# Kernel tuning notes

Measured on AMD Instinct MI355X. Metric: run time of the kernel, lower is better.

The kernel has to match this reference:

```python
import jax, jax.numpy as jnp
import numpy as np
from math import sqrt

B, T, C, H = 4, 2048, 1024, 16
D = C // H  # head dim = 64


def setup_inputs() -> dict:
    key = jax.random.key(0)
    ks = jax.random.split(key, 9)
    s = 1.0 / sqrt(C)
    return {
        "x": jax.random.normal(ks[0], (B, T, C), dtype=jnp.float32),
        "Wk": jax.random.normal(ks[1], (C, C), dtype=jnp.float32) * s,
        "bk": jax.random.normal(ks[2], (C,), dtype=jnp.float32) * 0.01,
        "Wq": jax.random.normal(ks[3], (C, C), dtype=jnp.float32) * s,
        "bq": jax.random.normal(ks[4], (C,), dtype=jnp.float32) * 0.01,
        "Wv": jax.random.normal(ks[5], (C, C), dtype=jnp.float32) * s,
        "bv": jax.random.normal(ks[6], (C,), dtype=jnp.float32) * 0.01,
        "Wp": jax.random.normal(ks[7], (C, C), dtype=jnp.float32) * s,
        "bp": jax.random.normal(ks[8], (C,), dtype=jnp.float32) * 0.01,
    }


def reference(x, Wk, bk, Wq, bq, Wv, bv, Wp, bp):
    # Linear projections, split into heads: [B, H, T, D]
    def heads(y):
        return y.reshape(B, T, H, D).transpose(0, 2, 1, 3)

    k = heads(x @ Wk + bk)
    q = heads(x @ Wq + bq)
    v = heads(x @ Wv + bv)

    # scaled dot-product attention with causal mask (dropout p=0 -> identity)
    attn = jnp.einsum("bhtd,bhsd->bhts", q, k) / jnp.sqrt(jnp.float32(D))
    causal = jnp.tril(jnp.ones((T, T), dtype=bool))
    attn = jnp.where(causal[None, None], attn, -jnp.inf)
    attn = jax.nn.softmax(attn, axis=-1)

    y = jnp.einsum("bhts,bhsd->bhtd", attn, v)  # [B, H, T, D]
    y = y.transpose(0, 2, 1, 3).reshape(B, T, C)
    return y @ Wp + bp
```

## Files before the change

### kernel.cpp

```cpp
#include <hip/hip_runtime.h>
#include <hip/hip_bf16.h>
#include <math.h>


typedef short bf16x8 __attribute__((ext_vector_type(8)));
typedef float f32x4 __attribute__((ext_vector_type(4)));
typedef _Float16 f16x4 __attribute__((ext_vector_type(4)));

__device__ __forceinline__ short f2b(float f) {
    unsigned u = __float_as_uint(f);
    u = (u + 0x7fffu + ((u >> 16) & 1u)) >> 16;
    return (short)u;
}
__device__ __forceinline__ float b2f(short s) {
    return __uint_as_float(((unsigned)(unsigned short)s) << 16);
}

__global__ __launch_bounds__(256) void cast_x_kernel(const float* __restrict__ x,
                                                     short* __restrict__ xb, int n4) {
    int idx = blockIdx.x * 256 + threadIdx.x;
    if (idx >= n4) return;
    float4 v = ((const float4*)x)[idx];
    short4 o;
    o.x = f2b(v.x); o.y = f2b(v.y); o.z = f2b(v.z); o.w = f2b(v.w);
    ((short4*)xb)[idx] = o;
}

__global__ __launch_bounds__(256) void wtrans_kernel(const float* W0, const float* W1,
                                                     const float* W2, const float* W3,
                                                     short* O0, short* O1, short* O2, short* O3) {
    const float* W; short* O;
    switch (blockIdx.z) {
        case 0: W = W0; O = O0; break;
        case 1: W = W1; O = O1; break;
        case 2: W = W2; O = O2; break;
        default: W = W3; O = O3; break;
    }
    __shared__ __align__(16) float Ls[64 * 68];
    int tid = threadIdx.x;
    int n0 = blockIdx.x * 64, k0 = blockIdx.y * 64;
    #pragma unroll
    for (int it = 0; it < 4; ++it) {
        int c = tid + it * 256;
        int r = c >> 4, off = (c & 15) * 4;
        *(float4*)&Ls[r * 68 + off] = *(const float4*)&W[(k0 + r) * 1024 + n0 + off];
    }
    __syncthreads();
    #pragma unroll
    for (int it = 0; it < 2; ++it) {
        int c = tid + it * 256;
        int n = c >> 3, koff = (c & 7) * 8;
        union { short s[8]; int4 v; } u;
        #pragma unroll
        for (int k = 0; k < 8; ++k) u.s[k] = f2b(Ls[(koff + k) * 68 + n]);
        *(int4*)&O[(n0 + n) * 1024 + k0 + koff] = u.v;
    }
}

template<int MODE>
__global__ __launch_bounds__(512, 2) void gemm8_kernel(const short* __restrict__ A,
                                                       const short* Bt0, const short* Bt1, const short* Bt2,
                                                       const float* b0, const float* b1, const float* b2,
                                                       float s0, float s1, float s2,
                                                       void* O0, void* O1, void* O2) {
    int z = blockIdx.z;
    const short* Bt   = (z == 0) ? Bt0 : (z == 1) ? Bt1 : Bt2;
    const float* bias = (z == 0) ? b0  : (z == 1) ? b1  : b2;
    float scl         = (z == 0) ? s0  : (z == 1) ? s1  : s2;
    void* Out         = (z == 0) ? O0  : (z == 1) ? O1  : O2;

    __shared__ __align__(16) short lds[73728];

    int tid = threadIdx.x;
    int w = tid >> 6, lane = tid & 63, quad = lane >> 4, l15 = lane & 15;
    int m0 = blockIdx.x * 128, n0 = blockIdx.y * 256;

    int srccol = ((lane & 3) * 8) ^ ((lane & 32) ? 16 : 0);
    const short* pA0 = A  + (m0 + w * 16 + (lane >> 2)) * 1024 + srccol;
    const short* pA1 = pA0 + 32;
    const short* pB0 = Bt + (n0 + (2 * w) * 16 + (lane >> 2)) * 1024 + srccol;
    const short* pB1 = pB0 + 32;
    const short* pB2 = pB0 + 16 * 1024;
    const short* pB3 = pB2 + 32;

    int dA = (w * 2) * 512;
    int dB = 24576 + (w * 4) * 512;

    int offR = l15 * 64 + ((quad * 16) ^ ((l15 & 8) << 2));
    int ma4 = (w >> 2) * 4;
    int nb2 = (w & 3) * 2;
    const char* ldsb = (const char*)lds;

    f32x4 acc[2][4][2] = {};

#define STG(p, off) __builtin_amdgcn_global_load_lds( \
        (const __attribute__((address_space(1))) unsigned int*)(p), \
        (__attribute__((address_space(3))) unsigned int*)&lds[off], 16, 0, 0)

    STG(pA0,      dA);                 STG(pA1,      dA + 512);
    STG(pB0,      dB);                 STG(pB1,      dB + 512);
    STG(pB2,      dB + 1024);          STG(pB3,      dB + 1536);
    STG(pA0 + 64, 8192 + dA);          STG(pA1 + 64, 8192 + dA + 512);
    STG(pB0 + 64, 16384 + dB);         STG(pB1 + 64, 16384 + dB + 512);
    STG(pB2 + 64, 16384 + dB + 1024);  STG(pB3 + 64, 16384 + dB + 1536);
    asm volatile("s_waitcnt vmcnt(6)" ::: "memory");
    __builtin_amdgcn_s_barrier();
    __builtin_amdgcn_sched_barrier(0);

    #pragma unroll
    for (int t = 0; t < 16; ++t) {
        const int rs = t % 3;
        const int ss = (t + 2) % 3;
        const int Ar = rs * 16384;
        const int Br = 49152 + rs * 32768;

        bf16x8 af[4][2], bf[2][2];
        #pragma unroll
        for (int i = 0; i < 4; ++i)
            #pragma unroll
            for (int kk = 0; kk < 2; ++kk)
                af[i][kk] = *(const bf16x8*)(ldsb + Ar + ((ma4 + i) * 2 + kk) * 1024 + offR);
        #pragma unroll
        for (int j = 0; j < 2; ++j)
            #pragma unroll
            for (int kk = 0; kk < 2; ++kk)
                bf[j][kk] = *(const bf16x8*)(ldsb + Br + ((nb2 + j) * 2 + kk) * 1024 + offR);
        if (t + 2 < 16) {
            STG(pA0 + (t + 2) * 64, ss * 8192 + dA);
            STG(pA1 + (t + 2) * 64, ss * 8192 + dA + 512);
            STG(pB0 + (t + 2) * 64, ss * 16384 + dB);
        }
        __builtin_amdgcn_s_barrier();
        asm volatile("s_waitcnt lgkmcnt(0)" ::: "memory");
        __builtin_amdgcn_sched_barrier(0);
        __builtin_amdgcn_s_setprio(1);
        #pragma unroll
        for (int i = 0; i < 4; ++i)
            #pragma unroll
            for (int j = 0; j < 2; ++j) {
                acc[0][i][j] = __builtin_amdgcn_mfma_f32_16x16x32_bf16(af[i][0], bf[j][0], acc[0][i][j], 0, 0, 0);
                acc[0][i][j] = __builtin_amdgcn_mfma_f32_16x16x32_bf16(af[i][1], bf[j][1], acc[0][i][j], 0, 0, 0);
            }
        __builtin_amdgcn_s_setprio(0);
        __builtin_amdgcn_s_barrier();
        __builtin_amdgcn_sched_barrier(0);

        #pragma unroll
        for (int j = 0; j < 2; ++j)
            #pragma unroll
            for (int kk = 0; kk < 2; ++kk)
                bf[j][kk] = *(const bf16x8*)(ldsb + Br + ((8 + nb2 + j) * 2 + kk) * 1024 + offR);
        if (t + 2 < 16) {
            STG(pB1 + (t + 2) * 64, ss * 16384 + dB + 512);
            STG(pB2 + (t + 2) * 64, ss * 16384 + dB + 1024);
            STG(pB3 + (t + 2) * 64, ss * 16384 + dB + 1536);
        }
        __builtin_amdgcn_s_barrier();
        asm volatile("s_waitcnt lgkmcnt(0)" ::: "memory");
        __builtin_amdgcn_sched_barrier(0);
        __builtin_amdgcn_s_setprio(1);
        #pragma unroll
        for (int i = 0; i < 4; ++i)
            #pragma unroll
            for (int j = 0; j < 2; ++j) {
                acc[1][i][j] = __builtin_amdgcn_mfma_f32_16x16x32_bf16(af[i][0], bf[j][0], acc[1][i][j], 0, 0, 0);
                acc[1][i][j] = __builtin_amdgcn_mfma_f32_16x16x32_bf16(af[i][1], bf[j][1], acc[1][i][j], 0, 0, 0);
            }
        __builtin_amdgcn_s_setprio(0);
        if (t < 14) {
            asm volatile("s_waitcnt vmcnt(6)" ::: "memory");
        } else if (t == 14) {
            asm volatile("s_waitcnt vmcnt(0)" ::: "memory");
        }
        if (t < 15) {
            __builtin_amdgcn_s_barrier();
            __builtin_amdgcn_sched_barrier(0);
        }
    }
#undef STG

    int mrow = m0 + (w >> 2) * 64;
    int ncol = n0 + (w & 3) * 32;
    #pragma unroll
    for (int nh = 0; nh < 2; ++nh) {
        #pragma unroll
        for (int i = 0; i < 4; ++i) {
            #pragma unroll
            for (int j = 0; j < 2; ++j) {
                int gn = ncol + nh * 128 + j * 16 + l15;
                float bv = bias[gn];
                #pragma unroll
                for (int r = 0; r < 4; ++r) {
                    int gm = mrow + i * 16 + quad * 4 + r;
                    float v = (acc[nh][i][j][r] + bv) * scl;
                    if (MODE == 0) {
                        int b = gm >> 11, tt = gm & 2047, h = gn >> 6, d = gn & 63;
                        ((short*)Out)[(((b * 16 + h) * 2048) + tt) * 64 + d] = f2b(v);
                    } else {
                        ((float*)Out)[gm * 1024 + gn] = v;
                    }
                }
            }
        }
    }
}

__global__ __launch_bounds__(256) void vtrans_kernel(const short* __restrict__ V,
                                                     _Float16* __restrict__ Vt) {
    __shared__ __align__(16) short Ts[64 * 72];
    int tid = threadIdx.x;
    int bh = blockIdx.y;
    int t0 = blockIdx.x * 64;
    #pragma unroll
    for (int it = 0; it < 2; ++it) {
        int c = tid + it * 256;
        int r = c >> 3, off = (c & 7) * 8;
        *(int4*)&Ts[r * 72 + off] = *(const int4*)&V[(bh * 2048 + t0 + r) * 64 + off];
    }
    __syncthreads();
    #pragma unroll
    for (int it = 0; it < 2; ++it) {
        int c = tid + it * 256;
        int d = c >> 3, toff = (c & 7) * 8;
        union { _Float16 h[8]; int4 v; } u;
        #pragma unroll
        for (int k = 0; k < 8; ++k) u.h[k] = (_Float16)b2f(Ts[(toff + k) * 72 + d]);
        *(int4*)&Vt[(bh * 64 + d) * 2048 + t0 + toff] = u.v;
    }
}

__global__ __launch_bounds__(256, 3) void attn_kernel(const short* __restrict__ Q,
                                                      const short* __restrict__ K,
                                                      const _Float16* __restrict__ Vt,
                                                      short* __restrict__ Y) {
    __shared__ __align__(16) short    Ks[128 * 64];
    __shared__ __align__(16) _Float16 Vs[64 * 128];

    int tid = threadIdx.x;
    int w = tid >> 6, lane = tid & 63, quad = lane >> 4, l15 = lane & 15;
    int idx = blockIdx.x;
    int qi = 15 - (idx >> 6);
    int bh = idx & 63;

    const short* Qh = Q + bh * 2048 * 64;
    const short* Kh = K + bh * 2048 * 64;
    const _Float16* Vh = Vt + bh * 64 * 2048;

    bf16x8 qf[2][2];
    #pragma unroll
    for (int i = 0; i < 2; ++i)
        #pragma unroll
        for (int kh = 0; kh < 2; ++kh) {
            int t = qi * 128 + w * 32 + i * 16 + l15;
            qf[i][kh] = *(const bf16x8*)&Qh[t * 64 + kh * 32 + quad * 8];
        }

    int krow = lane >> 3;
    int kchunk = ((lane & 7) ^ krow) * 8;
    int vrow = lane >> 4;
    int vchunk = ((lane & 15) ^ (w * 4 + vrow)) * 8;

    int t7 = l15 & 7;
    int kf0_off = ((quad ^ t7) * 8);
    int kf1_off = (((quad + 4) ^ t7) * 8);
    int vsub = (quad & 1) * 4;
    int vchi = quad >> 1;

    f32x4 o[2][4] = {};
    float lsum[2] = {0.f, 0.f};

    for (int si = 0; si <= qi; ++si) {
        const short* Kt = Kh + si * 128 * 64;
        const _Float16* Vtile = Vh + si * 128;
        bool diag = (si == qi);

        __syncthreads();
        #pragma unroll
        for (int it = 0; it < 4; ++it) {
            int kr0 = it * 32 + w * 8;
            __builtin_amdgcn_global_load_lds(
                (const __attribute__((address_space(1))) unsigned int*)&Kt[(kr0 + krow) * 64 + kchunk],
                (__attribute__((address_space(3))) unsigned int*)&Ks[kr0 * 64], 16, 0, 0);
            int vr0 = it * 16 + w * 4;
            __builtin_amdgcn_global_load_lds(
                (const __attribute__((address_space(1))) unsigned int*)&Vtile[(vr0 + vrow) * 2048 + vchunk],
                (__attribute__((address_space(3))) unsigned int*)&Vs[vr0 * 128], 16, 0, 0);
        }
        __syncthreads();

        #pragma unroll
        for (int j = 0; j < 8; ++j) {
            int trow = (j * 16 + l15) * 64;
            bf16x8 kf0 = *(const bf16x8*)&Ks[trow + kf0_off];
            bf16x8 kf1 = *(const bf16x8*)&Ks[trow + kf1_off];
            f16x4 pfv[2];
            #pragma unroll
            for (int i = 0; i < 2; ++i) {
                f32x4 a = {};
                a = __builtin_amdgcn_mfma_f32_16x16x32_bf16(kf0, qf[i][0], a, 0, 0, 0);
                a = __builtin_amdgcn_mfma_f32_16x16x32_bf16(kf1, qf[i][1], a, 0, 0, 0);
                if (diag) {
                    int qrel = w * 32 + i * 16 + l15;
                    #pragma unroll
                    for (int r = 0; r < 4; ++r)
                        if (j * 16 + quad * 4 + r > qrel) a[r] = -1e30f;
                }
                float p0 = __builtin_amdgcn_exp2f(a[0]);
                float p1 = __builtin_amdgcn_exp2f(a[1]);
                float p2 = __builtin_amdgcn_exp2f(a[2]);
                float p3 = __builtin_amdgcn_exp2f(a[3]);
                lsum[i] += (p0 + p1) + (p2 + p3);
                pfv[i][0] = (_Float16)p0;
                pfv[i][1] = (_Float16)p1;
                pfv[i][2] = (_Float16)p2;
                pfv[i][3] = (_Float16)p3;
            }
            int vc = (j * 2 + vchi);
            #pragma unroll
            for (int mt = 0; mt < 4; ++mt) {
                int d = mt * 16 + l15;
                f16x4 vf = *(const f16x4*)&Vs[d * 128 + ((vc ^ l15) * 8) + vsub];
                o[0][mt] = __builtin_amdgcn_mfma_f32_16x16x16f16(vf, pfv[0], o[0][mt], 0, 0, 0);
                o[1][mt] = __builtin_amdgcn_mfma_f32_16x16x16f16(vf, pfv[1], o[1][mt], 0, 0, 0);
            }
        }
    }

    int b = bh >> 4, h = bh & 15;
    #pragma unroll
    for (int i = 0; i < 2; ++i) {
        float l = lsum[i];
        l += __shfl_xor(l, 16);
        l += __shfl_xor(l, 32);
        float rinv = 1.0f / l;
        int q = qi * 128 + w * 32 + i * 16 + l15;
        short* yrow = &Y[(b * 2048 + q) * 1024 + h * 64];
        #pragma unroll
        for (int mt = 0; mt < 4; ++mt) {
            short4 s4;
            s4.x = f2b(o[i][mt][0] * rinv);
            s4.y = f2b(o[i][mt][1] * rinv);
            s4.z = f2b(o[i][mt][2] * rinv);
            s4.w = f2b(o[i][mt][3] * rinv);
            *(short4*)&yrow[mt * 16 + quad * 4] = s4;
        }
    }
}

extern "C" void kernel_launch(void* const* d_in, const int* in_sizes, int n_in,
                              void* d_out, int out_size, void* d_ws, size_t ws_size,
                              hipStream_t stream) {
    const float* x  = (const float*)d_in[0];
    const float* Wk = (const float*)d_in[1];
    const float* bk = (const float*)d_in[2];
    const float* Wq = (const float*)d_in[3];
    const float* bq = (const float*)d_in[4];
    const float* Wv = (const float*)d_in[5];
    const float* bv = (const float*)d_in[6];
    const float* Wp = (const float*)d_in[7];
    const float* bp = (const float*)d_in[8];

    char* ws = (char*)d_ws;
    short*     xb  = (short*)(ws + 0);
    short*     Wqt = (short*)(ws + 16777216);
    short*     Wkt = (short*)(ws + 18874368);
    short*     Wvt = (short*)(ws + 20971520);
    short*     Wpt = (short*)(ws + 23068672);
    short*     Qb  = (short*)(ws + 25165824);
    short*     Kb  = (short*)(ws + 41943040);
    short*     Vb  = (short*)(ws + 58720256);
    _Float16*  Vtb = (_Float16*)(ws + 75497472);
    short*     Yb  = (short*)(ws + 92274688);

    cast_x_kernel<<<8192, 256, 0, stream>>>(x, xb, 2097152);
    wtrans_kernel<<<dim3(16, 16, 4), 256, 0, stream>>>(Wq, Wk, Wv, Wp, Wqt, Wkt, Wvt, Wpt);
    gemm8_kernel<0><<<dim3(64, 4, 3), 512, 0, stream>>>(xb, Wqt, Wkt, Wvt, bq, bk, bv,
                                                        0.18033688011112042f , 1.0f, 1.0f,
                                                        (void*)Qb, (void*)Kb, (void*)Vb);
    vtrans_kernel<<<dim3(32, 64), 256, 0, stream>>>(Vb, Vtb);
    attn_kernel<<<1024, 256, 0, stream>>>(Qb, Kb, Vtb, Yb);
    gemm8_kernel<1><<<dim3(64, 4, 1), 512, 0, stream>>>(Yb, Wpt, nullptr, nullptr,
                                                        bp, nullptr, nullptr,
                                                        1.0f, 1.0f, 1.0f,
                                                        (void*)d_out, nullptr, nullptr);
}
```

Measured before the change: 241.9 us.

## Software-pipeline LDS fragment reads across k-halves in GEMM main loop

Restructures the GEMM inner loop so the wave splits each 64-wide k-step into two 32-wide halves. Fragments for the next half are read from LDS while MFMAs run on the current half, using double-buffered register sets and partial lgkmcnt waits. This removes one barrier per half-step and reorders the accumulators into a single 4x4 grid. The cost is more live VGPRs and more fragile waitcnt and barrier ordering around the triple-buffered LDS stages.

```diff
diff --git a/kernel.cpp b/kernel.cpp
--- a/kernel.cpp
+++ b/kernel.cpp
@@ -89,13 +89,17 @@
     int offR = l15 * 64 + ((quad * 16) ^ ((l15 & 8) << 2));
     int ma4 = (w >> 2) * 4;
     int nb2 = (w & 3) * 2;
+    int jrow0 = nb2, jrow1 = nb2 + 1, jrow2 = nb2 + 8, jrow3 = nb2 + 9;
     const char* ldsb = (const char*)lds;
 
-    f32x4 acc[2][4][2] = {};
+    f32x4 acc[4][4] = {};
+
+    bf16x8 afA[4], bfA[4], afB[4], bfB[4];
 
 #define STG(p, off) __builtin_amdgcn_global_load_lds( \
         (const __attribute__((address_space(1))) unsigned int*)(p), \
         (__attribute__((address_space(3))) unsigned int*)&lds[off], 16, 0, 0)
+#define RD(base, row, kk) (*(const bf16x8*)(ldsb + (base) + ((row) * 2 + (kk)) * 1024 + offR))
 
     STG(pA0,      dA);                 STG(pA1,      dA + 512);
     STG(pB0,      dB);                 STG(pB1,      dB + 512);
@@ -108,97 +112,95 @@
     __builtin_amdgcn_sched_barrier(0);
 
     #pragma unroll
+    for (int i = 0; i < 4; ++i) afA[i] = RD(0, ma4 + i, 0);
+    bfA[0] = RD(49152, jrow0, 0); bfA[1] = RD(49152, jrow1, 0);
+    bfA[2] = RD(49152, jrow2, 0); bfA[3] = RD(49152, jrow3, 0);
+
+    #pragma unroll
     for (int t = 0; t < 16; ++t) {
-        const int rs = t % 3;
-        const int ss = (t + 2) % 3;
-        const int Ar = rs * 16384;
-        const int Br = 49152 + rs * 32768;
-
-        bf16x8 af[4][2], bf[2][2];
-        #pragma unroll
-        for (int i = 0; i < 4; ++i)
-            #pragma unroll
-            for (int kk = 0; kk < 2; ++kk)
-                af[i][kk] = *(const bf16x8*)(ldsb + Ar + ((ma4 + i) * 2 + kk) * 1024 + offR);
-        #pragma unroll
-        for (int j = 0; j < 2; ++j)
-            #pragma unroll
-            for (int kk = 0; kk < 2; ++kk)
-                bf[j][kk] = *(const bf16x8*)(ldsb + Br + ((nb2 + j) * 2 + kk) * 1024 + offR);
+        const int rs  = t % 3;
+        const int rs1 = (t + 1) % 3;
+        const int ss  = (t + 2) % 3;
+        const int Ar  = rs * 16384;
+        const int Br  = 49152 + rs * 32768;
+        const int Ar1 = rs1 * 16384;
+        const int Br1 = 49152 + rs1 * 32768;
+
+        #pragma unroll
+        for (int i = 0; i < 4; ++i) afB[i] = RD(Ar, ma4 + i, 1);
+        bfB[0] = RD(Br, jrow0, 1); bfB[1] = RD(Br, jrow1, 1);
+        bfB[2] = RD(Br, jrow2, 1); bfB[3] = RD(Br, jrow3, 1);
         if (t + 2 < 16) {
             STG(pA0 + (t + 2) * 64, ss * 8192 + dA);
             STG(pA1 + (t + 2) * 64, ss * 8192 + dA + 512);
             STG(pB0 + (t + 2) * 64, ss * 16384 + dB);
         }
-        __builtin_amdgcn_s_barrier();
-        asm volatile("s_waitcnt lgkmcnt(0)" ::: "memory");
+        asm volatile("s_waitcnt lgkmcnt(8)" ::: "memory");
         __builtin_amdgcn_sched_barrier(0);
         __builtin_amdgcn_s_setprio(1);
         #pragma unroll
         for (int i = 0; i < 4; ++i)
             #pragma unroll
-            for (int j = 0; j < 2; ++j) {
-                acc[0][i][j] = __builtin_amdgcn_mfma_f32_16x16x32_bf16(af[i][0], bf[j][0], acc[0][i][j], 0, 0, 0);
-                acc[0][i][j] = __builtin_amdgcn_mfma_f32_16x16x32_bf16(af[i][1], bf[j][1], acc[0][i][j], 0, 0, 0);
-            }
+            for (int j = 0; j < 4; ++j)
+                acc[i][j] = __builtin_amdgcn_mfma_f32_16x16x32_bf16(afA[i], bfA[j], acc[i][j], 0, 0, 0);
         __builtin_amdgcn_s_setprio(0);
+        if (t < 14) {
+            asm volatile("s_waitcnt vmcnt(3)" ::: "memory");
+        } else if (t == 14) {
+            asm volatile("s_waitcnt vmcnt(0)" ::: "memory");
+        }
         __builtin_amdgcn_s_barrier();
         __builtin_amdgcn_sched_barrier(0);
 
-        #pragma unroll
-        for (int j = 0; j < 2; ++j)
-            #pragma unroll
-            for (int kk = 0; kk < 2; ++kk)
-                bf[j][kk] = *(const bf16x8*)(ldsb + Br + ((8 + nb2 + j) * 2 + kk) * 1024 + offR);
+        if (t < 15) {
+            #pragma unroll
+            for (int i = 0; i < 4; ++i) afA[i] = RD(Ar1, ma4 + i, 0);
+            bfA[0] = RD(Br1, jrow0, 0); bfA[1] = RD(Br1, jrow1, 0);
+            bfA[2] = RD(Br1, jrow2, 0); bfA[3] = RD(Br1, jrow3, 0);
+        }
         if (t + 2 < 16) {
             STG(pB1 + (t + 2) * 64, ss * 16384 + dB + 512);
             STG(pB2 + (t + 2) * 64, ss * 16384 + dB + 1024);
             STG(pB3 + (t + 2) * 64, ss * 16384 + dB + 1536);
         }
-        __builtin_amdgcn_s_barrier();
-        asm volatile("s_waitcnt lgkmcnt(0)" ::: "memory");
+        if (t < 15) {
+            asm volatile("s_waitcnt lgkmcnt(8)" ::: "memory");
+        } else {
+            asm volatile("s_waitcnt lgkmcnt(0)" ::: "memory");
+        }
         __builtin_amdgcn_sched_barrier(0);
         __builtin_amdgcn_s_setprio(1);
         #pragma unroll
         for (int i = 0; i < 4; ++i)
             #pragma unroll
-            for (int j = 0; j < 2; ++j) {
-                acc[1][i][j] = __builtin_amdgcn_mfma_f32_16x16x32_bf16(af[i][0], bf[j][0], acc[1][i][j], 0, 0, 0);
-                acc[1][i][j] = __builtin_amdgcn_mfma_f32_16x16x32_bf16(af[i][1], bf[j][1], acc[1][i][j], 0, 0, 0);
-            }
+            for (int j = 0; j < 4; ++j)
+                acc[i][j] = __builtin_amdgcn_mfma_f32_16x16x32_bf16(afB[i], bfB[j], acc[i][j], 0, 0, 0);
         __builtin_amdgcn_s_setprio(0);
-        if (t < 14) {
-            asm volatile("s_waitcnt vmcnt(6)" ::: "memory");
-        } else if (t == 14) {
-            asm volatile("s_waitcnt vmcnt(0)" ::: "memory");
-        }
         if (t < 15) {
             __builtin_amdgcn_s_barrier();
             __builtin_amdgcn_sched_barrier(0);
         }
     }
 #undef STG
+#undef RD
 
     int mrow = m0 + (w >> 2) * 64;
     int ncol = n0 + (w & 3) * 32;
     #pragma unroll
-    for (int nh = 0; nh < 2; ++nh) {
-        #pragma unroll
-        for (int i = 0; i < 4; ++i) {
-            #pragma unroll
-            for (int j = 0; j < 2; ++j) {
-                int gn = ncol + nh * 128 + j * 16 + l15;
-                float bv = bias[gn];
-                #pragma unroll
-                for (int r = 0; r < 4; ++r) {
-                    int gm = mrow + i * 16 + quad * 4 + r;
-                    float v = (acc[nh][i][j][r] + bv) * scl;
-                    if (MODE == 0) {
-                        int b = gm >> 11, tt = gm & 2047, h = gn >> 6, d = gn & 63;
-                        ((short*)Out)[(((b * 16 + h) * 2048) + tt) * 64 + d] = f2b(v);
-                    } else {
-                        ((float*)Out)[gm * 1024 + gn] = v;
-                    }
+    for (int i = 0; i < 4; ++i) {
+        #pragma unroll
+        for (int j = 0; j < 4; ++j) {
+            int gn = ncol + (j >> 1) * 128 + (j & 1) * 16 + l15;
+            float bv = bias[gn];
+            #pragma unroll
+            for (int r = 0; r < 4; ++r) {
+                int gm = mrow + i * 16 + quad * 4 + r;
+                float v = (acc[i][j][r] + bv) * scl;
+                if (MODE == 0) {
+                    int b = gm >> 11, tt = gm & 2047, h = gn >> 6, d = gn & 63;
+                    ((short*)Out)[(((b * 16 + h) * 2048) + tt) * 64 + d] = f2b(v);
+                } else {
+                    ((float*)Out)[gm * 1024 + gn] = v;
                 }
             }
         }
```

Result: no change. 242.5 us (+0.3%).
